# Optimization experiments

Hardware: AMD Instinct MI355X
Metric: run time of the kernel (lower is better)

## Reference

```python
import jax, jax.numpy as jnp
import numpy as np

K = 3  # hardcoded kNN size in the module

def setup_inputs() -> dict:
    key = jax.random.key(0)
    ks = jax.random.split(key, 8)
    B, M, N, C, NC, OUT = 2, 4096, 8192, 512, 20, 512
    def rn(k, sh, sc=1.0):
        return jax.random.normal(k, sh, dtype=jnp.float32) * sc
    return {
        "src_points": rn(ks[0], (B, M, 3)),
        "tgt_points": rn(ks[1], (B, N, 3)),
        "src_features": rn(ks[2], (B, M, C)),
        # semantic_head: Linear(C,128) -> ReLU -> Linear(128,NC)
        "w_sem1": rn(ks[3], (C, 128), 0.04), "b_sem1": jnp.zeros((128,), jnp.float32),
        "w_sem2": rn(ks[4], (128, NC), 0.08), "b_sem2": jnp.zeros((NC,), jnp.float32),
        # upsample_net: Linear(C+NC,256) -> ReLU -> Linear(256,OUT)
        "w_up1": rn(ks[5], (C + NC, 256), 0.04), "b_up1": jnp.zeros((256,), jnp.float32),
        "w_up2": rn(ks[6], (256, OUT), 0.06), "b_up2": jnp.zeros((OUT,), jnp.float32),
    }

def reference(src_points, tgt_points, src_features,
              w_sem1, b_sem1, w_sem2, b_sem2,
              w_up1, b_up1, w_up2, b_up2):
    # semantic logits per source point: [B, M, NC]
    semantic_logits = jax.nn.relu(src_features @ w_sem1 + b_sem1) @ w_sem2 + b_sem2
    # pairwise euclidean distances tgt->src: [B, N, M]
    d2 = (jnp.sum(tgt_points * tgt_points, -1)[:, :, None]
          + jnp.sum(src_points * src_points, -1)[:, None, :]
          - 2.0 * jnp.einsum('bnd,bmd->bnm', tgt_points, src_points))
    dists = jnp.sqrt(jnp.maximum(d2, 0.0))
    # k smallest distances and their indices
    neg_vals, knn_idx = jax.lax.top_k(-dists, K)   # [B, N, K]
    knn_d = -neg_vals                               # gathered distances, [B, N, K]
    # gather neighbor features / semantics: [B, N, K, C] and [B, N, K, NC]
    knn_features = jax.vmap(lambda f, i: f[i])(src_features, knn_idx)
    knn_semantic = jax.vmap(lambda f, i: f[i])(semantic_logits, knn_idx)
    # inverse-distance softmax weights over the K neighbors
    weights = jax.nn.softmax(-knn_d, axis=-1)                       # [B, N, K]
    semantic_weights = jax.nn.softmax(knn_semantic, axis=-1).mean(axis=2)  # [B, N, NC]
    fused_features = jnp.einsum('bnkd,bnk->bnd', knn_features, weights)    # [B, N, C]
    combined = jnp.concatenate([fused_features, semantic_weights], axis=-1)
    upsampled = jax.nn.relu(combined @ w_up1 + b_up1) @ w_up2 + b_up2      # [B, N, OUT]
    return (upsampled, semantic_logits)
```

## Files before the change

kernel.cpp:

```cpp
#include <hip/hip_runtime.h>
#include <math.h>

#define BB 2
#define MM 4096
#define NN 8192
#define CC 512
#define NC 20
#define OUTD 512
#define H1 128
#define H2 256
#define CIN 532
#define KNN 3
#define SPLIT 8
#define CHUNK (MM / SPLIT)
#define QTR (CHUNK / 4)

#define RR 32
#define CS1 552
#define HS 264
#define KT1 17
#define KT2 8

#define FS 520
#define HS2 136
#define SKT1 16
#define SKT2 4

typedef __attribute__((ext_vector_type(8))) short s8;
typedef __attribute__((ext_vector_type(4))) float f4;

__device__ inline unsigned short f2bf(float x) {
    unsigned u = __float_as_uint(x);
    unsigned r = (u + 0x7FFFu + ((u >> 16) & 1u)) >> 16;
    return (unsigned short)r;
}
__device__ inline float bf2f(unsigned short u) {
    return __uint_as_float(((unsigned)u) << 16);
}

__global__ __launch_bounds__(256) void prep_kernel(
    const float* __restrict__ srcp,
    const float* __restrict__ wu1, const float* __restrict__ wu2,
    const float* __restrict__ ws1, const float* __restrict__ ws2,
    float4* __restrict__ sp4,
    unsigned short* __restrict__ w1p, unsigned short* __restrict__ w2p,
    unsigned short* __restrict__ ws1p, unsigned short* __restrict__ ws2p)
{
    int i = blockIdx.x * 256 + threadIdx.x;
    if (i < BB * MM) {
        float x = srcp[(size_t)i * 3 + 0];
        float y = srcp[(size_t)i * 3 + 1];
        float z = srcp[(size_t)i * 3 + 2];
        sp4[i] = make_float4(x, y, z, x * x + y * y + z * z);
    }
    if (i < KT1 * H2 * 32) {
        int kk = i & 31, n = (i >> 5) & 255, kb = i >> 13;
        int k = kb * 32 + kk;
        w1p[i] = f2bf((k < CIN) ? wu1[(size_t)k * H2 + n] : 0.0f);
    }
    if (i < KT2 * OUTD * 32) {
        int kk = i & 31, n = (i >> 5) & 511, kb = i >> 14;
        int k = kb * 32 + kk;
        w2p[i] = f2bf(wu2[(size_t)k * OUTD + n]);
    }
    if (i < SKT1 * H1 * 32) {
        int kk = i & 31, n = (i >> 5) & 127, kb = i >> 12;
        int k = kb * 32 + kk;
        ws1p[i] = f2bf(ws1[(size_t)k * H1 + n]);
    }
    if (i < SKT2 * 32 * 32) {
        int kk = i & 31, n = (i >> 5) & 31, kb = i >> 10;
        int k = kb * 32 + kk;
        ws2p[i] = f2bf((n < NC) ? ws2[(size_t)k * NC + n] : 0.0f);
    }
}

__global__ __launch_bounds__(256) void sem_kernel(
    const float* __restrict__ feat,
    const unsigned short* __restrict__ ws1p, const unsigned short* __restrict__ ws2p,
    const float* __restrict__ b1g, const float* __restrict__ b2g,
    float* __restrict__ logits_out, unsigned short* __restrict__ P)
{
    __shared__ unsigned short sfeat[32 * FS];
    __shared__ unsigned short shid[32 * HS2];
    __shared__ float slg[32][33];
    const int tid = threadIdx.x;
    const int row0 = blockIdx.x * 32;
    const int lane = tid & 63;
    const int wv = tid >> 6;
    const int l15 = lane & 15;
    const int quad = lane >> 4;

    {
        const int r = tid >> 3, p = tid & 7;
        const float4* fr = (const float4*)(feat + (size_t)(row0 + r) * CC);
#pragma unroll 4
        for (int j = 0; j < 16; ++j) {
            int c4 = j * 8 + p;
            float4 a = fr[c4];
            ushort4 s;
            s.x = f2bf(a.x); s.y = f2bf(a.y); s.z = f2bf(a.z); s.w = f2bf(a.w);
            *(ushort4*)&sfeat[r * FS + c4 * 4] = s;
        }
    }
    __syncthreads();

    {
        const int n0 = wv * 32;
        f4 acc[2][2];
#pragma unroll
        for (int rt = 0; rt < 2; ++rt)
#pragma unroll
            for (int c = 0; c < 2; ++c) acc[rt][c] = (f4){0.f, 0.f, 0.f, 0.f};
        for (int kb = 0; kb < SKT1; ++kb) {
            s8 a0 = *(const s8*)&sfeat[l15 * FS + kb * 32 + quad * 8];
            s8 a1 = *(const s8*)&sfeat[(l15 + 16) * FS + kb * 32 + quad * 8];
#pragma unroll
            for (int c = 0; c < 2; ++c) {
                s8 bf = *(const s8*)&ws1p[((size_t)(kb * H1 + n0 + c * 16 + l15)) * 32 + quad * 8];
                acc[0][c] = __builtin_amdgcn_mfma_f32_16x16x32_bf16(a0, bf, acc[0][c], 0, 0, 0);
                acc[1][c] = __builtin_amdgcn_mfma_f32_16x16x32_bf16(a1, bf, acc[1][c], 0, 0, 0);
            }
        }
#pragma unroll
        for (int c = 0; c < 2; ++c) {
            int col = n0 + c * 16 + l15;
            float bias = b1g[col];
#pragma unroll
            for (int rt = 0; rt < 2; ++rt)
#pragma unroll
                for (int i = 0; i < 4; ++i) {
                    int rr = rt * 16 + quad * 4 + i;
                    shid[rr * HS2 + col] = f2bf(fmaxf(acc[rt][c][i] + bias, 0.0f));
                }
        }
    }
    __syncthreads();

    {
        const int rt = wv & 1, ct = wv >> 1;
        f4 acc2 = (f4){0.f, 0.f, 0.f, 0.f};
        for (int kb = 0; kb < SKT2; ++kb) {
            s8 a = *(const s8*)&shid[(rt * 16 + l15) * HS2 + kb * 32 + quad * 8];
            s8 bf = *(const s8*)&ws2p[((size_t)(kb * 32 + ct * 16 + l15)) * 32 + quad * 8];
            acc2 = __builtin_amdgcn_mfma_f32_16x16x32_bf16(a, bf, acc2, 0, 0, 0);
        }
        int col = ct * 16 + l15;
        float bias = (col < NC) ? b2g[col] : 0.0f;
#pragma unroll
        for (int i = 0; i < 4; ++i) {
            int rr = rt * 16 + quad * 4 + i;
            float v = acc2[i] + bias;
            slg[rr][col] = v;
            if (col < NC)
                logits_out[(size_t)(row0 + rr) * NC + col] = v;
        }
    }
    __syncthreads();

    if (tid < 32) {
        int r = tid;
        float mx = -1e30f;
        for (int nc = 0; nc < NC; ++nc) mx = fmaxf(mx, slg[r][nc]);
        float s = 0.0f;
        float e[NC];
#pragma unroll
        for (int nc = 0; nc < NC; ++nc) { e[nc] = __expf(slg[r][nc] - mx); s += e[nc]; }
        float inv = 1.0f / s;
#pragma unroll
        for (int nc = 0; nc < NC; ++nc)
            P[(size_t)(row0 + r) * NC + nc] = f2bf(e[nc] * inv);
    }
}

__global__ __launch_bounds__(256) void knn_partial(
    const float4* __restrict__ sp4, const float* __restrict__ tgtp,
    float* __restrict__ pd2, unsigned short* __restrict__ pidx)
{
    __shared__ float4 pts[CHUNK];
    const int tid = threadIdx.x;
    const int t = blockIdx.x * 256 + tid;
    const int bu = blockIdx.x >> 5;
    const int chunk = blockIdx.y;
    const int mbase = chunk * CHUNK;
    const float4* sp = sp4 + (size_t)bu * MM + mbase;
    for (int i = tid; i < CHUNK; i += 256) pts[i] = sp[i];
    __syncthreads();

    const float tx = tgtp[(size_t)t * 3 + 0];
    const float ty = tgtp[(size_t)t * 3 + 1];
    const float tz = tgtp[(size_t)t * 3 + 2];
    const float m2x = -2.0f * tx, m2y = -2.0f * ty, m2z = -2.0f * tz;

    float b0[4], b1[4], b2[4];
    int i0[4], i1[4], i2[4];
#pragma unroll
    for (int k = 0; k < 4; ++k) {
        b0[k] = b1[k] = b2[k] = 1e30f;
        i0[k] = i1[k] = i2[k] = 0;
    }

#pragma unroll 2
    for (int m = 0; m < QTR; ++m) {
#pragma unroll
        for (int k = 0; k < 4; ++k) {
            float4 p = pts[k * QTR + m];
            float d = fmaf(m2x, p.x, fmaf(m2y, p.y, fmaf(m2z, p.z, p.w)));
            int mi = mbase + k * QTR + m;
            bool l2 = d < b2[k], l1 = d < b1[k], l0 = d < b0[k];
            b2[k] = l1 ? b1[k] : (l2 ? d : b2[k]); i2[k] = l1 ? i1[k] : (l2 ? mi : i2[k]);
            b1[k] = l0 ? b0[k] : (l1 ? d : b1[k]); i1[k] = l0 ? i0[k] : (l1 ? mi : i1[k]);
            b0[k] = l0 ? d : b0[k];                i0[k] = l0 ? mi : i0[k];
        }
    }
#pragma unroll
    for (int k = 1; k < 4; ++k) {
#pragma unroll
        for (int j = 0; j < 3; ++j) {
            float d = (j == 0) ? b0[k] : (j == 1) ? b1[k] : b2[k];
            int   i = (j == 0) ? i0[k] : (j == 1) ? i1[k] : i2[k];
            bool e2 = d < b2[0], e1 = d < b1[0], e0 = d < b0[0];
            b2[0] = e1 ? b1[0] : (e2 ? d : b2[0]); i2[0] = e1 ? i1[0] : (e2 ? i : i2[0]);
            b1[0] = e0 ? b0[0] : (e1 ? d : b1[0]); i1[0] = e0 ? i0[0] : (e1 ? i : i1[0]);
            b0[0] = e0 ? d : b0[0];                i0[0] = e0 ? i : i0[0];
        }
    }
    size_t o = ((size_t)t * SPLIT + chunk) * KNN;
    pd2[o + 0] = b0[0]; pd2[o + 1] = b1[0]; pd2[o + 2] = b2[0];
    pidx[o + 0] = (unsigned short)i0[0];
    pidx[o + 1] = (unsigned short)i1[0];
    pidx[o + 2] = (unsigned short)i2[0];
}

__global__ __launch_bounds__(256) void up_kernel(
    const float* __restrict__ feat, const unsigned short* __restrict__ P,
    const float* __restrict__ pd2, const unsigned short* __restrict__ pidx,
    const float* __restrict__ tgtp,
    const unsigned short* __restrict__ w1p, const unsigned short* __restrict__ w2p,
    const float* __restrict__ b1g, const float* __restrict__ b2g,
    float* __restrict__ out)
{
    __shared__ unsigned short comb[RR * CS1];
    __shared__ unsigned short hid[RR * HS];
    __shared__ float sg[RR][3];
    __shared__ int   sj[RR][3];
    const int tid = threadIdx.x;
    const int row0 = blockIdx.x * RR;
    const int lane = tid & 63;
    const int wv = tid >> 6;
    const int l15 = lane & 15;
    const int quad = lane >> 4;

    if (tid < RR) {
        int row = row0 + tid;
        float b0 = 1e30f, b1 = 1e30f, b2 = 1e30f;
        int i0 = 0, i1 = 0, i2 = 0;
        size_t base = (size_t)row * SPLIT * KNN;
#pragma unroll
        for (int j = 0; j < SPLIT * KNN; ++j) {
            float d = pd2[base + j];
            int m = pidx[base + j];
            bool l2 = d < b2, l1 = d < b1, l0 = d < b0;
            b2 = l1 ? b1 : (l2 ? d : b2); i2 = l1 ? i1 : (l2 ? m : i2);
            b1 = l0 ? b0 : (l1 ? d : b1); i1 = l0 ? i0 : (l1 ? m : i1);
            b0 = l0 ? d : b0;             i0 = l0 ? m : i0;
        }
        float tx = tgtp[(size_t)row * 3 + 0];
        float ty = tgtp[(size_t)row * 3 + 1];
        float tz = tgtp[(size_t)row * 3 + 2];
        float t2 = tx * tx + ty * ty + tz * tz;
        float d0 = sqrtf(fmaxf(b0 + t2, 0.0f));
        float d1 = sqrtf(fmaxf(b1 + t2, 0.0f));
        float d2v = sqrtf(fmaxf(b2 + t2, 0.0f));
        float e1 = __expf(d0 - d1);
        float e2 = __expf(d0 - d2v);
        float inv = 1.0f / (1.0f + e1 + e2);
        sg[tid][0] = inv; sg[tid][1] = e1 * inv; sg[tid][2] = e2 * inv;
        sj[tid][0] = i0; sj[tid][1] = i1; sj[tid][2] = i2;
    }
    __syncthreads();

    {
        const int r = tid >> 3, p = tid & 7;
        int row = row0 + r;
        int b = row >> 13;
        int j0 = sj[r][0], j1 = sj[r][1], j2 = sj[r][2];
        float g0 = sg[r][0], g1 = sg[r][1], g2 = sg[r][2];
        const float* F = feat + (size_t)b * MM * CC;
        const float4* f0 = (const float4*)(F + (size_t)j0 * CC);
        const float4* f1 = (const float4*)(F + (size_t)j1 * CC);
        const float4* f2 = (const float4*)(F + (size_t)j2 * CC);
#pragma unroll 4
        for (int j = 0; j < 16; ++j) {
            int c4 = j * 8 + p;
            float4 a0 = f0[c4], a1 = f1[c4], a2 = f2[c4];
            ushort4 s;
            s.x = f2bf(g0 * a0.x + g1 * a1.x + g2 * a2.x);
            s.y = f2bf(g0 * a0.y + g1 * a1.y + g2 * a2.y);
            s.z = f2bf(g0 * a0.z + g1 * a1.z + g2 * a2.z);
            s.w = f2bf(g0 * a0.w + g1 * a1.w + g2 * a2.w);
            *(ushort4*)&comb[r * CS1 + c4 * 4] = s;
        }
        const unsigned short* Pb = P + (size_t)b * MM * NC;
        if (p < 4) {
            for (int q = p; q < 32; q += 4) {
                unsigned short v = 0;
                if (q < NC)
                    v = f2bf((bf2f(Pb[(size_t)j0 * NC + q]) + bf2f(Pb[(size_t)j1 * NC + q]) +
                              bf2f(Pb[(size_t)j2 * NC + q])) * (1.0f / 3.0f));
                comb[r * CS1 + 512 + q] = v;
            }
        }
    }
    __syncthreads();

    {
        const int n0 = wv * 64;
        f4 acc1[2][4];
#pragma unroll
        for (int rt = 0; rt < 2; ++rt)
#pragma unroll
            for (int c = 0; c < 4; ++c) acc1[rt][c] = (f4){0.f, 0.f, 0.f, 0.f};
        for (int kb = 0; kb < KT1; ++kb) {
            s8 a0 = *(const s8*)&comb[l15 * CS1 + kb * 32 + quad * 8];
            s8 a1 = *(const s8*)&comb[(l15 + 16) * CS1 + kb * 32 + quad * 8];
            s8 bfr[4];
#pragma unroll
            for (int c = 0; c < 4; ++c)
                bfr[c] = *(const s8*)&w1p[((size_t)(kb * H2 + n0 + c * 16 + l15)) * 32 + quad * 8];
#pragma unroll
            for (int c = 0; c < 4; ++c) {
                acc1[0][c] = __builtin_amdgcn_mfma_f32_16x16x32_bf16(a0, bfr[c], acc1[0][c], 0, 0, 0);
                acc1[1][c] = __builtin_amdgcn_mfma_f32_16x16x32_bf16(a1, bfr[c], acc1[1][c], 0, 0, 0);
            }
        }
#pragma unroll
        for (int c = 0; c < 4; ++c) {
            int ccol = n0 + c * 16 + l15;
            float bias = b1g[ccol];
#pragma unroll
            for (int rt = 0; rt < 2; ++rt)
#pragma unroll
                for (int i = 0; i < 4; ++i) {
                    int rr = rt * 16 + quad * 4 + i;
                    hid[rr * HS + ccol] = f2bf(fmaxf(acc1[rt][c][i] + bias, 0.0f));
                }
        }
    }
    __syncthreads();

    {
        const int m0 = wv * 128;
        f4 acc2[2][8];
#pragma unroll
        for (int rt = 0; rt < 2; ++rt)
#pragma unroll
            for (int c = 0; c < 8; ++c) acc2[rt][c] = (f4){0.f, 0.f, 0.f, 0.f};
        for (int kb = 0; kb < KT2; ++kb) {
            s8 a0 = *(const s8*)&hid[l15 * HS + kb * 32 + quad * 8];
            s8 a1 = *(const s8*)&hid[(l15 + 16) * HS + kb * 32 + quad * 8];
            s8 bfr[8];
#pragma unroll
            for (int c = 0; c < 8; ++c)
                bfr[c] = *(const s8*)&w2p[((size_t)(kb * OUTD + m0 + c * 16 + l15)) * 32 + quad * 8];
#pragma unroll
            for (int c = 0; c < 8; ++c) {
                acc2[0][c] = __builtin_amdgcn_mfma_f32_16x16x32_bf16(a0, bfr[c], acc2[0][c], 0, 0, 0);
                acc2[1][c] = __builtin_amdgcn_mfma_f32_16x16x32_bf16(a1, bfr[c], acc2[1][c], 0, 0, 0);
            }
        }
#pragma unroll
        for (int c = 0; c < 8; ++c) {
            int ccol = m0 + c * 16 + l15;
            float bias = b2g[ccol];
#pragma unroll
            for (int rt = 0; rt < 2; ++rt)
#pragma unroll
                for (int i = 0; i < 4; ++i) {
                    int rr = rt * 16 + quad * 4 + i;
                    out[(size_t)(row0 + rr) * OUTD + ccol] = acc2[rt][c][i] + bias;
                }
        }
    }
}

extern "C" void kernel_launch(void* const* d_in, const int* in_sizes, int n_in,
                              void* d_out, int out_size, void* d_ws, size_t ws_size,
                              hipStream_t stream) {
    (void)in_sizes; (void)n_in; (void)out_size; (void)ws_size;
    const float* src_points   = (const float*)d_in[0];
    const float* tgt_points   = (const float*)d_in[1];
    const float* src_features = (const float*)d_in[2];
    const float* w_sem1 = (const float*)d_in[3];
    const float* b_sem1 = (const float*)d_in[4];
    const float* w_sem2 = (const float*)d_in[5];
    const float* b_sem2 = (const float*)d_in[6];
    const float* w_up1  = (const float*)d_in[7];
    const float* b_up1  = (const float*)d_in[8];
    const float* w_up2  = (const float*)d_in[9];
    const float* b_up2  = (const float*)d_in[10];

    float* out    = (float*)d_out;
    float* ups    = out;
    float* logits = out + (size_t)BB * NN * OUTD;

    char* w = (char*)d_ws;
    float4* sp4 = (float4*)w;                          w += (size_t)BB * MM * 16;
    float* pd2  = (float*)w;                           w += (size_t)BB * NN * SPLIT * KNN * 4;
    unsigned short* P    = (unsigned short*)w;         w += (size_t)BB * MM * NC * 2;
    unsigned short* pidx = (unsigned short*)w;         w += (size_t)BB * NN * SPLIT * KNN * 2;
    unsigned short* w1p  = (unsigned short*)w;         w += (size_t)KT1 * H2 * 32 * 2;
    unsigned short* w2p  = (unsigned short*)w;         w += (size_t)KT2 * OUTD * 32 * 2;
    unsigned short* ws1p = (unsigned short*)w;         w += (size_t)SKT1 * H1 * 32 * 2;
    unsigned short* ws2p = (unsigned short*)w;         w += (size_t)SKT2 * 32 * 32 * 2;

    prep_kernel<<<dim3((KT1 * H2 * 32 + 255) / 256), dim3(256), 0, stream>>>(
        src_points, w_up1, w_up2, w_sem1, w_sem2, sp4, w1p, w2p, ws1p, ws2p);
    sem_kernel<<<dim3(BB * MM / 32), dim3(256), 0, stream>>>(
        src_features, ws1p, ws2p, b_sem1, b_sem2, logits, P);
    knn_partial<<<dim3(BB * NN / 256, SPLIT), dim3(256), 0, stream>>>(
        sp4, tgt_points, pd2, pidx);
    up_kernel<<<dim3(BB * NN / RR), dim3(256), 0, stream>>>(
        src_features, P, pd2, pidx, tgt_points, w1p, w2p, b_up1, b_up2, ups);
}
```

Measured before the change: 168.3 us.

## Precompute first upsample layer per source point and interpolate projected features

Uses linearity of the first upsample Linear to project each source point's features (and its semantic softmax) through w_up1 once in the semantic kernel, storing a 512-wide bf16 table T per source point. The upsample kernel then forms the hidden pre-activation as a weighted sum of three gathered rows of T instead of gathering 512-dim features and running a 532x256 GEMM per target point. This roughly halves first-layer GEMM work, since there are half as many source points as targets, and shrinks the gather. The cost is an extra 8 MB intermediate and an extra bf16 rounding of the projected values. The kNN split is also doubled to 16 chunks for more parallelism, at the price of more partial candidates to merge.

```diff
diff --git a/kernel.cpp b/kernel.cpp
--- a/kernel.cpp
+++ b/kernel.cpp
@@ -11,18 +11,19 @@
 #define H2 256
 #define CIN 532
 #define KNN 3
-#define SPLIT 8
+#define SPLIT 16
 #define CHUNK (MM / SPLIT)
-#define QTR (CHUNK / 4)
+#define CLEN (CHUNK / 4)
 
 #define RR 32
-#define CS1 552
 #define HS 264
 #define KT1 17
 #define KT2 8
 
+#define RO 16
 #define FS 520
 #define HS2 136
+#define TS 512
 #define SKT1 16
 #define SKT2 4
 
@@ -36,6 +37,9 @@
 }
 __device__ inline float bf2f(unsigned short u) {
     return __uint_as_float(((unsigned)u) << 16);
+}
+__device__ inline float bf2fs(short u) {
+    return __uint_as_float(((unsigned)(unsigned short)u) << 16);
 }
 
 __global__ __launch_bounds__(256) void prep_kernel(
@@ -78,25 +82,28 @@
 __global__ __launch_bounds__(256) void sem_kernel(
     const float* __restrict__ feat,
     const unsigned short* __restrict__ ws1p, const unsigned short* __restrict__ ws2p,
-    const float* __restrict__ b1g, const float* __restrict__ b2g,
-    float* __restrict__ logits_out, unsigned short* __restrict__ P)
+    const unsigned short* __restrict__ w1p,
+    const float* __restrict__ b1s, const float* __restrict__ b2s,
+    float* __restrict__ logits_out, unsigned short* __restrict__ T)
 {
-    __shared__ unsigned short sfeat[32 * FS];
-    __shared__ unsigned short shid[32 * HS2];
-    __shared__ float slg[32][33];
+    __shared__ unsigned short sfeat[RO * FS];
+    __shared__ unsigned short Tst[RO * TS];
+    __shared__ unsigned short shid[RO * HS2];
+    __shared__ float slg[RO][33];
+    __shared__ unsigned short pP[RO * 32];
     const int tid = threadIdx.x;
-    const int row0 = blockIdx.x * 32;
+    const int row0 = blockIdx.x * RO;
     const int lane = tid & 63;
     const int wv = tid >> 6;
     const int l15 = lane & 15;
     const int quad = lane >> 4;
 
     {
-        const int r = tid >> 3, p = tid & 7;
+        const int r = tid >> 4, p = tid & 15;
         const float4* fr = (const float4*)(feat + (size_t)(row0 + r) * CC);
-#pragma unroll 4
-        for (int j = 0; j < 16; ++j) {
-            int c4 = j * 8 + p;
+#pragma unroll
+        for (int j = 0; j < 8; ++j) {
+            int c4 = j * 16 + p;
             float4 a = fr[c4];
             ushort4 s;
             s.x = f2bf(a.x); s.y = f2bf(a.y); s.z = f2bf(a.z); s.w = f2bf(a.w);
@@ -106,51 +113,59 @@
     __syncthreads();
 
     {
-        const int n0 = wv * 32;
-        f4 acc[2][2];
-#pragma unroll
-        for (int rt = 0; rt < 2; ++rt)
-#pragma unroll
-            for (int c = 0; c < 2; ++c) acc[rt][c] = (f4){0.f, 0.f, 0.f, 0.f};
+        f4 asem[2], ah[4];
+#pragma unroll
+        for (int c = 0; c < 2; ++c) asem[c] = (f4){0.f, 0.f, 0.f, 0.f};
+#pragma unroll
+        for (int c = 0; c < 4; ++c) ah[c] = (f4){0.f, 0.f, 0.f, 0.f};
         for (int kb = 0; kb < SKT1; ++kb) {
-            s8 a0 = *(const s8*)&sfeat[l15 * FS + kb * 32 + quad * 8];
-            s8 a1 = *(const s8*)&sfeat[(l15 + 16) * FS + kb * 32 + quad * 8];
+            s8 a = *(const s8*)&sfeat[l15 * FS + kb * 32 + quad * 8];
 #pragma unroll
             for (int c = 0; c < 2; ++c) {
-                s8 bf = *(const s8*)&ws1p[((size_t)(kb * H1 + n0 + c * 16 + l15)) * 32 + quad * 8];
-                acc[0][c] = __builtin_amdgcn_mfma_f32_16x16x32_bf16(a0, bf, acc[0][c], 0, 0, 0);
-                acc[1][c] = __builtin_amdgcn_mfma_f32_16x16x32_bf16(a1, bf, acc[1][c], 0, 0, 0);
+                s8 b = *(const s8*)&ws1p[((size_t)(kb * H1 + wv * 32 + c * 16 + l15)) * 32 + quad * 8];
+                asem[c] = __builtin_amdgcn_mfma_f32_16x16x32_bf16(a, b, asem[c], 0, 0, 0);
+            }
+#pragma unroll
+            for (int c = 0; c < 4; ++c) {
+                s8 b = *(const s8*)&w1p[((size_t)(kb * H2 + wv * 64 + c * 16 + l15)) * 32 + quad * 8];
+                ah[c] = __builtin_amdgcn_mfma_f32_16x16x32_bf16(a, b, ah[c], 0, 0, 0);
             }
         }
 #pragma unroll
         for (int c = 0; c < 2; ++c) {
-            int col = n0 + c * 16 + l15;
-            float bias = b1g[col];
-#pragma unroll
-            for (int rt = 0; rt < 2; ++rt)
-#pragma unroll
-                for (int i = 0; i < 4; ++i) {
-                    int rr = rt * 16 + quad * 4 + i;
-                    shid[rr * HS2 + col] = f2bf(fmaxf(acc[rt][c][i] + bias, 0.0f));
-                }
-        }
-    }
-    __syncthreads();
-
-    {
-        const int rt = wv & 1, ct = wv >> 1;
-        f4 acc2 = (f4){0.f, 0.f, 0.f, 0.f};
+            int col = wv * 32 + c * 16 + l15;
+            float bias = b1s[col];
+#pragma unroll
+            for (int i = 0; i < 4; ++i) {
+                int rr = quad * 4 + i;
+                shid[rr * HS2 + col] = f2bf(fmaxf(asem[c][i] + bias, 0.0f));
+            }
+        }
+#pragma unroll
+        for (int c = 0; c < 4; ++c) {
+            int col = wv * 64 + c * 16 + l15;
+#pragma unroll
+            for (int i = 0; i < 4; ++i) {
+                int rr = quad * 4 + i;
+                Tst[rr * TS + col] = f2bf(ah[c][i]);
+            }
+        }
+    }
+    __syncthreads();
+
+    if (wv < 2) {
+        f4 acc = (f4){0.f, 0.f, 0.f, 0.f};
         for (int kb = 0; kb < SKT2; ++kb) {
-            s8 a = *(const s8*)&shid[(rt * 16 + l15) * HS2 + kb * 32 + quad * 8];
-            s8 bf = *(const s8*)&ws2p[((size_t)(kb * 32 + ct * 16 + l15)) * 32 + quad * 8];
-            acc2 = __builtin_amdgcn_mfma_f32_16x16x32_bf16(a, bf, acc2, 0, 0, 0);
-        }
-        int col = ct * 16 + l15;
-        float bias = (col < NC) ? b2g[col] : 0.0f;
+            s8 a = *(const s8*)&shid[l15 * HS2 + kb * 32 + quad * 8];
+            s8 b = *(const s8*)&ws2p[((size_t)(kb * 32 + wv * 16 + l15)) * 32 + quad * 8];
+            acc = __builtin_amdgcn_mfma_f32_16x16x32_bf16(a, b, acc, 0, 0, 0);
+        }
+        int col = wv * 16 + l15;
+        float bias = (col < NC) ? b2s[col] : 0.0f;
 #pragma unroll
         for (int i = 0; i < 4; ++i) {
-            int rr = rt * 16 + quad * 4 + i;
-            float v = acc2[i] + bias;
+            int rr = quad * 4 + i;
+            float v = acc[i] + bias;
             slg[rr][col] = v;
             if (col < NC)
                 logits_out[(size_t)(row0 + rr) * NC + col] = v;
@@ -158,7 +173,7 @@
     }
     __syncthreads();
 
-    if (tid < 32) {
+    if (tid < RO) {
         int r = tid;
         float mx = -1e30f;
         for (int nc = 0; nc < NC; ++nc) mx = fmaxf(mx, slg[r][nc]);
@@ -168,8 +183,36 @@
         for (int nc = 0; nc < NC; ++nc) { e[nc] = __expf(slg[r][nc] - mx); s += e[nc]; }
         float inv = 1.0f / s;
 #pragma unroll
-        for (int nc = 0; nc < NC; ++nc)
-            P[(size_t)(row0 + r) * NC + nc] = f2bf(e[nc] * inv);
+        for (int nc = 0; nc < 32; ++nc)
+            pP[r * 32 + nc] = (nc < NC) ? f2bf(e[nc] * inv) : 0;
+    }
+    __syncthreads();
+
+    {
+        s8 a = *(const s8*)&pP[l15 * 32 + quad * 8];
+#pragma unroll
+        for (int c = 0; c < 4; ++c) {
+            s8 b = *(const s8*)&w1p[((size_t)(16 * H2 + wv * 64 + c * 16 + l15)) * 32 + quad * 8];
+            f4 acc = (f4){0.f, 0.f, 0.f, 0.f};
+            acc = __builtin_amdgcn_mfma_f32_16x16x32_bf16(a, b, acc, 0, 0, 0);
+            int col = wv * 64 + c * 16 + l15;
+#pragma unroll
+            for (int i = 0; i < 4; ++i) {
+                int rr = quad * 4 + i;
+                Tst[rr * TS + 256 + col] = f2bf(acc[i]);
+            }
+        }
+    }
+    __syncthreads();
+
+    {
+#pragma unroll
+        for (int v = 0; v < 4; ++v) {
+            int e = (tid + v * 256) * 8;
+            int r = e >> 9, c = e & (TS - 1);
+            s8 d = *(const s8*)&Tst[e];
+            *(s8*)&T[((size_t)(row0 + r)) * TS + c] = d;
+        }
     }
 }
 
@@ -184,7 +227,7 @@
     const int chunk = blockIdx.y;
     const int mbase = chunk * CHUNK;
     const float4* sp = sp4 + (size_t)bu * MM + mbase;
-    for (int i = tid; i < CHUNK; i += 256) pts[i] = sp[i];
+    pts[tid] = sp[tid];
     __syncthreads();
 
     const float tx = tgtp[(size_t)t * 3 + 0];
@@ -201,12 +244,12 @@
     }
 
 #pragma unroll 2
-    for (int m = 0; m < QTR; ++m) {
+    for (int m = 0; m < CLEN; ++m) {
 #pragma unroll
         for (int k = 0; k < 4; ++k) {
-            float4 p = pts[k * QTR + m];
+            float4 p = pts[k * CLEN + m];
             float d = fmaf(m2x, p.x, fmaf(m2y, p.y, fmaf(m2z, p.z, p.w)));
-            int mi = mbase + k * QTR + m;
+            int mi = mbase + k * CLEN + m;
             bool l2 = d < b2[k], l1 = d < b1[k], l0 = d < b0[k];
             b2[k] = l1 ? b1[k] : (l2 ? d : b2[k]); i2[k] = l1 ? i1[k] : (l2 ? mi : i2[k]);
             b1[k] = l0 ? b0[k] : (l1 ? d : b1[k]); i1[k] = l0 ? i0[k] : (l1 ? mi : i1[k]);
@@ -233,14 +276,13 @@
 }
 
 __global__ __launch_bounds__(256) void up_kernel(
-    const float* __restrict__ feat, const unsigned short* __restrict__ P,
+    const unsigned short* __restrict__ T,
     const float* __restrict__ pd2, const unsigned short* __restrict__ pidx,
     const float* __restrict__ tgtp,
-    const unsigned short* __restrict__ w1p, const unsigned short* __restrict__ w2p,
+    const unsigned short* __restrict__ w2p,
     const float* __restrict__ b1g, const float* __restrict__ b2g,
     float* __restrict__ out)
 {
-    __shared__ unsigned short comb[RR * CS1];
     __shared__ unsigned short hid[RR * HS];
     __shared__ float sg[RR][3];
     __shared__ int   sj[RR][3];
@@ -281,70 +323,31 @@
     __syncthreads();
 
     {
-        const int r = tid >> 3, p = tid & 7;
+        const int r = tid >> 3, p = tid & 7, c0 = p * 32;
         int row = row0 + r;
-        int b = row >> 13;
-        int j0 = sj[r][0], j1 = sj[r][1], j2 = sj[r][2];
-        float g0 = sg[r][0], g1 = sg[r][1], g2 = sg[r][2];
-        const float* F = feat + (size_t)b * MM * CC;
-        const float4* f0 = (const float4*)(F + (size_t)j0 * CC);
-        const float4* f1 = (const float4*)(F + (size_t)j1 * CC);
-        const float4* f2 = (const float4*)(F + (size_t)j2 * CC);
-#pragma unroll 4
-        for (int j = 0; j < 16; ++j) {
-            int c4 = j * 8 + p;
-            float4 a0 = f0[c4], a1 = f1[c4], a2 = f2[c4];
-            ushort4 s;
-            s.x = f2bf(g0 * a0.x + g1 * a1.x + g2 * a2.x);
-            s.y = f2bf(g0 * a0.y + g1 * a1.y + g2 * a2.y);
-            s.z = f2bf(g0 * a0.z + g1 * a1.z + g2 * a2.z);
-            s.w = f2bf(g0 * a0.w + g1 * a1.w + g2 * a2.w);
-            *(ushort4*)&comb[r * CS1 + c4 * 4] = s;
-        }
-        const unsigned short* Pb = P + (size_t)b * MM * NC;
-        if (p < 4) {
-            for (int q = p; q < 32; q += 4) {
-                unsigned short v = 0;
-                if (q < NC)
-                    v = f2bf((bf2f(Pb[(size_t)j0 * NC + q]) + bf2f(Pb[(size_t)j1 * NC + q]) +
-                              bf2f(Pb[(size_t)j2 * NC + q])) * (1.0f / 3.0f));
-                comb[r * CS1 + 512 + q] = v;
-            }
-        }
-    }
-    __syncthreads();
-
-    {
-        const int n0 = wv * 64;
-        f4 acc1[2][4];
-#pragma unroll
-        for (int rt = 0; rt < 2; ++rt)
-#pragma unroll
-            for (int c = 0; c < 4; ++c) acc1[rt][c] = (f4){0.f, 0.f, 0.f, 0.f};
-        for (int kb = 0; kb < KT1; ++kb) {
-            s8 a0 = *(const s8*)&comb[l15 * CS1 + kb * 32 + quad * 8];
-            s8 a1 = *(const s8*)&comb[(l15 + 16) * CS1 + kb * 32 + quad * 8];
-            s8 bfr[4];
-#pragma unroll
-            for (int c = 0; c < 4; ++c)
-                bfr[c] = *(const s8*)&w1p[((size_t)(kb * H2 + n0 + c * 16 + l15)) * 32 + quad * 8];
-#pragma unroll
-            for (int c = 0; c < 4; ++c) {
-                acc1[0][c] = __builtin_amdgcn_mfma_f32_16x16x32_bf16(a0, bfr[c], acc1[0][c], 0, 0, 0);
-                acc1[1][c] = __builtin_amdgcn_mfma_f32_16x16x32_bf16(a1, bfr[c], acc1[1][c], 0, 0, 0);
-            }
-        }
-#pragma unroll
-        for (int c = 0; c < 4; ++c) {
-            int ccol = n0 + c * 16 + l15;
-            float bias = b1g[ccol];
-#pragma unroll
-            for (int rt = 0; rt < 2; ++rt)
-#pragma unroll
-                for (int i = 0; i < 4; ++i) {
-                    int rr = rt * 16 + quad * 4 + i;
-                    hid[rr * HS + ccol] = f2bf(fmaxf(acc1[rt][c][i] + bias, 0.0f));
+        size_t bofs = (size_t)(row >> 13) * MM;
+        float pre[32];
+#pragma unroll
+        for (int cc = 0; cc < 32; ++cc) pre[cc] = 0.0f;
+#pragma unroll
+        for (int k = 0; k < 3; ++k) {
+            const unsigned short* Tr = T + (bofs + (size_t)sj[r][k]) * TS;
+            float gk = sg[r][k];
+#pragma unroll
+            for (int v = 0; v < 4; ++v) {
+                s8 h = *(const s8*)&Tr[c0 + v * 8];
+                s8 g = *(const s8*)&Tr[256 + c0 + v * 8];
+#pragma unroll
+                for (int e = 0; e < 8; ++e) {
+                    pre[v * 8 + e] = fmaf(gk, bf2fs(h[e]), pre[v * 8 + e]);
+                    pre[v * 8 + e] = fmaf(1.0f / 3.0f, bf2fs(g[e]), pre[v * 8 + e]);
                 }
+            }
+        }
+#pragma unroll
+        for (int cc = 0; cc < 32; ++cc) {
+            int c = c0 + cc;
+            hid[r * HS + c] = f2bf(fmaxf(pre[cc] + b1g[c], 0.0f));
         }
     }
     __syncthreads();
@@ -405,21 +408,21 @@
     float* logits = out + (size_t)BB * NN * OUTD;
 
     char* w = (char*)d_ws;
-    float4* sp4 = (float4*)w;                          w += (size_t)BB * MM * 16;
-    float* pd2  = (float*)w;                           w += (size_t)BB * NN * SPLIT * KNN * 4;
-    unsigned short* P    = (unsigned short*)w;         w += (size_t)BB * MM * NC * 2;
-    unsigned short* pidx = (unsigned short*)w;         w += (size_t)BB * NN * SPLIT * KNN * 2;
-    unsigned short* w1p  = (unsigned short*)w;         w += (size_t)KT1 * H2 * 32 * 2;
-    unsigned short* w2p  = (unsigned short*)w;         w += (size_t)KT2 * OUTD * 32 * 2;
-    unsigned short* ws1p = (unsigned short*)w;         w += (size_t)SKT1 * H1 * 32 * 2;
-    unsigned short* ws2p = (unsigned short*)w;         w += (size_t)SKT2 * 32 * 32 * 2;
+    float4* sp4 = (float4*)w;                  w += (size_t)BB * MM * 16;
+    unsigned short* T = (unsigned short*)w;    w += (size_t)BB * MM * TS * 2;
+    float* pd2  = (float*)w;                   w += (size_t)BB * NN * SPLIT * KNN * 4;
+    unsigned short* pidx = (unsigned short*)w; w += (size_t)BB * NN * SPLIT * KNN * 2;
+    unsigned short* w1p  = (unsigned short*)w; w += (size_t)KT1 * H2 * 32 * 2;
+    unsigned short* w2p  = (unsigned short*)w; w += (size_t)KT2 * OUTD * 32 * 2;
+    unsigned short* ws1p = (unsigned short*)w; w += (size_t)SKT1 * H1 * 32 * 2;
+    unsigned short* ws2p = (unsigned short*)w; w += (size_t)SKT2 * 32 * 32 * 2;
 
     prep_kernel<<<dim3((KT1 * H2 * 32 + 255) / 256), dim3(256), 0, stream>>>(
         src_points, w_up1, w_up2, w_sem1, w_sem2, sp4, w1p, w2p, ws1p, ws2p);
-    sem_kernel<<<dim3(BB * MM / 32), dim3(256), 0, stream>>>(
-        src_features, ws1p, ws2p, b_sem1, b_sem2, logits, P);
+    sem_kernel<<<dim3(BB * MM / RO), dim3(256), 0, stream>>>(
+        src_features, ws1p, ws2p, w1p, b_sem1, b_sem2, logits, T);
     knn_partial<<<dim3(BB * NN / 256, SPLIT), dim3(256), 0, stream>>>(
         sp4, tgt_points, pd2, pidx);
     up_kernel<<<dim3(BB * NN / RR), dim3(256), 0, stream>>>(
-        src_features, P, pd2, pidx, tgt_points, w1p, w2p, b_up1, b_up2, ups);
-}
+        T, pd2, pidx, tgt_points, w2p, b_up1, b_up2, ups);
+}
```

Result: no change. 168.7 us (+0.2%).
